# Performance work log

Hardware: AMD Instinct MI355X
Metric: run time of the kernel (lower is better)

## Reference

```python
import jax, jax.numpy as jnp
import numpy as np

B, P, PLOIDY = 8, 5000, 2
NALLELES, NPOS, D = 16, 20000, 64


def setup_inputs() -> dict:
    key = jax.random.key(0)
    k1, k2, k3, k4, k5 = jax.random.split(key, 5)
    alleles = jax.random.randint(k1, (B, P, PLOIDY), 0, NALLELES, dtype=jnp.int32)
    positions = jax.random.randint(k2, (B, P), 0, NPOS, dtype=jnp.int32)
    allele_table = jax.random.normal(k3, (NALLELES, D), dtype=jnp.float32)
    kernel_table = jax.random.normal(k4, (NPOS, D * D), dtype=jnp.float32)
    bias_table = jax.random.normal(k5, (NPOS, D), dtype=jnp.float32)
    return {"alleles": alleles, "positions": positions,
            "allele_table": allele_table, "kernel_table": kernel_table,
            "bias_table": bias_table}


def reference(alleles, positions, allele_table, kernel_table, bias_table):
    # gather allele embeddings and sum over ploidy: [B,P,ploidy,D] -> [B,P,D]
    a = allele_table[alleles].sum(axis=-2)
    # per-position weight matrix: [B,P,D,D]
    kernel = kernel_table[positions].reshape(positions.shape[0], positions.shape[1], D, D)
    bias = bias_table[positions]                       # [B,P,D]
    # batched 1xD @ DxD matmul, fused with bias add
    out = jnp.einsum('bpd,bpde->bpe', a, kernel) + bias
    return out  # activation is None (linear)
```

## Files before the change

### kernel.cpp

```cpp
#include <hip/hip_runtime.h>

#define BB 8
#define PP 5000
#define DD 64
#define NBP (BB * PP)
#define NPOSC 20000
#define SLOTS 16
#define GRID_POS (NPOSC / 4)

static __device__ __forceinline__ float4 f4add(float4 a, float4 b) {
    return make_float4(a.x + b.x, a.y + b.y, a.z + b.z, a.w + b.w);
}

__global__ __launch_bounds__(256) void claim_kernel(
    const int* __restrict__ positions,
    int* __restrict__ cnt,
    int* __restrict__ ovf_cnt,
    int* __restrict__ order2,
    int* __restrict__ ovf)
{
    const int tid = blockIdx.x * 256 + threadIdx.x;
    if (tid < NBP) {
        const int p = positions[tid];
        const int k = atomicAdd(&cnt[p], 1);
        if (k < SLOTS) order2[p * SLOTS + k] = tid;
        else           ovf[atomicAdd(ovf_cnt, 1)] = tid;
    }
}

__global__ __launch_bounds__(256) void allele_embed_kernel(
    const int* __restrict__ alleles,
    const float* __restrict__ allele_table,
    const float4* __restrict__ ktab4,
    const float4* __restrict__ btab4,
    const int* __restrict__ cnt,
    const int* __restrict__ order2,
    float4* __restrict__ out4)
{
    const int wave = threadIdx.x >> 6;
    const int lane = threadIdx.x & 63;
    const int work = (blockIdx.x & 7) * (GRID_POS / 8) + (blockIdx.x >> 3);
    const int pos  = work * 4 + wave;

    int n = cnt[pos];
    if (n == 0) return;
    if (n > SLOTS) n = SLOTS;

    const float4* __restrict__ krow = ktab4 + (size_t)pos * (DD * DD / 4);
    const int* __restrict__ slot = order2 + pos * SLOTS;
    const int dg = lane >> 4;
    const float4 bv = btab4[(size_t)pos * (DD / 4) + (lane & 15)];

    if (n == 1) {
        const int bp = slot[0];
        const float a = allele_table[alleles[bp * 2] * DD + lane]
                      + allele_table[alleles[bp * 2 + 1] * DD + lane];
        float4 acc = make_float4(0.f, 0.f, 0.f, 0.f);
#pragma unroll
        for (int i = 0; i < 16; ++i) {
            const float ad = __shfl(a, i * 4 + dg, 64);
            const float4 kv = krow[i * 64 + lane];
            acc.x += ad * kv.x; acc.y += ad * kv.y;
            acc.z += ad * kv.z; acc.w += ad * kv.w;
        }
#pragma unroll
        for (int off = 16; off <= 32; off <<= 1) {
            acc.x += __shfl_xor(acc.x, off, 64); acc.y += __shfl_xor(acc.y, off, 64);
            acc.z += __shfl_xor(acc.z, off, 64); acc.w += __shfl_xor(acc.w, off, 64);
        }
        if (lane < 16) out4[(size_t)bp * (DD / 4) + lane] = f4add(acc, bv);
        return;
    }

    for (int c = 0; c < n; c += 4) {
        const int m = n - c;
        const int bp0 = slot[c];
        const int bp1 = (m > 1) ? slot[c + 1] : bp0;
        const int bp2 = (m > 2) ? slot[c + 2] : bp0;
        const int bp3 = (m > 3) ? slot[c + 3] : bp0;

        const float a0 = allele_table[alleles[bp0 * 2] * DD + lane]
                       + allele_table[alleles[bp0 * 2 + 1] * DD + lane];
        const float a1 = allele_table[alleles[bp1 * 2] * DD + lane]
                       + allele_table[alleles[bp1 * 2 + 1] * DD + lane];
        const float a2 = allele_table[alleles[bp2 * 2] * DD + lane]
                       + allele_table[alleles[bp2 * 2 + 1] * DD + lane];
        const float a3 = allele_table[alleles[bp3 * 2] * DD + lane]
                       + allele_table[alleles[bp3 * 2 + 1] * DD + lane];

        float4 acc0 = make_float4(0.f, 0.f, 0.f, 0.f);
        float4 acc1 = acc0, acc2 = acc0, acc3 = acc0;
#pragma unroll
        for (int i = 0; i < 16; ++i) {
            const int d = i * 4 + dg;
            const float4 kv = krow[i * 64 + lane];
            const float d0 = __shfl(a0, d, 64);
            const float d1 = __shfl(a1, d, 64);
            const float d2 = __shfl(a2, d, 64);
            const float d3 = __shfl(a3, d, 64);
            acc0.x += d0 * kv.x; acc0.y += d0 * kv.y; acc0.z += d0 * kv.z; acc0.w += d0 * kv.w;
            acc1.x += d1 * kv.x; acc1.y += d1 * kv.y; acc1.z += d1 * kv.z; acc1.w += d1 * kv.w;
            acc2.x += d2 * kv.x; acc2.y += d2 * kv.y; acc2.z += d2 * kv.z; acc2.w += d2 * kv.w;
            acc3.x += d3 * kv.x; acc3.y += d3 * kv.y; acc3.z += d3 * kv.z; acc3.w += d3 * kv.w;
        }
#pragma unroll
        for (int off = 16; off <= 32; off <<= 1) {
            acc0.x += __shfl_xor(acc0.x, off, 64); acc0.y += __shfl_xor(acc0.y, off, 64);
            acc0.z += __shfl_xor(acc0.z, off, 64); acc0.w += __shfl_xor(acc0.w, off, 64);
            acc1.x += __shfl_xor(acc1.x, off, 64); acc1.y += __shfl_xor(acc1.y, off, 64);
            acc1.z += __shfl_xor(acc1.z, off, 64); acc1.w += __shfl_xor(acc1.w, off, 64);
            acc2.x += __shfl_xor(acc2.x, off, 64); acc2.y += __shfl_xor(acc2.y, off, 64);
            acc2.z += __shfl_xor(acc2.z, off, 64); acc2.w += __shfl_xor(acc2.w, off, 64);
            acc3.x += __shfl_xor(acc3.x, off, 64); acc3.y += __shfl_xor(acc3.y, off, 64);
            acc3.z += __shfl_xor(acc3.z, off, 64); acc3.w += __shfl_xor(acc3.w, off, 64);
        }
        if (lane < 16) {
            out4[(size_t)bp0 * (DD / 4) + lane] = f4add(acc0, bv);
            if (m > 1) out4[(size_t)bp1 * (DD / 4) + lane] = f4add(acc1, bv);
            if (m > 2) out4[(size_t)bp2 * (DD / 4) + lane] = f4add(acc2, bv);
            if (m > 3) out4[(size_t)bp3 * (DD / 4) + lane] = f4add(acc3, bv);
        }
    }
}

__global__ __launch_bounds__(256) void tail_kernel(
    const int* __restrict__ alleles,
    const int* __restrict__ positions,
    const float* __restrict__ allele_table,
    const float4* __restrict__ ktab4,
    const float4* __restrict__ btab4,
    const int* __restrict__ ovf_cnt,
    const int* __restrict__ ovf,
    float4* __restrict__ out4)
{
    const int nov  = *ovf_cnt;
    const int lane = threadIdx.x & 63;
    const int wid  = blockIdx.x * 4 + (threadIdx.x >> 6);
    const int dg   = lane >> 4;
    for (int i = wid; i < nov; i += 256) {
        const int bp  = ovf[i];
        const int pos = positions[bp];
        const float a = allele_table[alleles[bp * 2] * DD + lane]
                      + allele_table[alleles[bp * 2 + 1] * DD + lane];
        const float4* krow = ktab4 + (size_t)pos * (DD * DD / 4);
        float4 acc = make_float4(0.f, 0.f, 0.f, 0.f);
#pragma unroll
        for (int k = 0; k < 16; ++k) {
            const float ad = __shfl(a, k * 4 + dg, 64);
            const float4 kv = krow[k * 64 + lane];
            acc.x += ad * kv.x; acc.y += ad * kv.y;
            acc.z += ad * kv.z; acc.w += ad * kv.w;
        }
#pragma unroll
        for (int off = 16; off <= 32; off <<= 1) {
            acc.x += __shfl_xor(acc.x, off, 64); acc.y += __shfl_xor(acc.y, off, 64);
            acc.z += __shfl_xor(acc.z, off, 64); acc.w += __shfl_xor(acc.w, off, 64);
        }
        if (lane < 16) {
            const float4 bv = btab4[(size_t)pos * (DD / 4) + lane];
            out4[(size_t)bp * (DD / 4) + lane] = f4add(acc, bv);
        }
    }
}

extern "C" void kernel_launch(void* const* d_in, const int* in_sizes, int n_in,
                              void* d_out, int out_size, void* d_ws, size_t ws_size,
                              hipStream_t stream) {
    const int*   alleles      = (const int*)d_in[0];
    const int*   positions    = (const int*)d_in[1];
    const float* allele_table = (const float*)d_in[2];
    const float4* ktab4       = (const float4*)d_in[3];
    const float4* btab4       = (const float4*)d_in[4];
    float4* out4              = (float4*)d_out;

    int* cnt     = (int*)d_ws;
    int* ovf_cnt = cnt + NPOSC;
    int* order2  = cnt + NPOSC + 32;
    int* ovf     = order2 + NPOSC * SLOTS;

    hipMemsetAsync(cnt, 0, (NPOSC + 32) * sizeof(int), stream);

    const int gprep = (NBP + 255) / 256;
    claim_kernel<<<gprep, 256, 0, stream>>>(positions, cnt, ovf_cnt, order2, ovf);

    allele_embed_kernel<<<GRID_POS, 256, 0, stream>>>(
        alleles, allele_table, ktab4, btab4, cnt, order2, out4);

    tail_kernel<<<64, 256, 0, stream>>>(
        alleles, positions, allele_table, ktab4, btab4, ovf_cnt, ovf, out4);
}
```

Before: 442.6 us.

## Use nontemporal kernel-table loads and output stores, vector types, and paired claims

Streams the per-position weight rows and the output with nontemporal loads and stores so they bypass cache retention, and switches to native ext_vector float4 arithmetic. Reads the allele pairs as a single int2 load. The claim kernel now handles two positions per thread, and the tail kernel is shrunk to 16 blocks with a matching stride. Nontemporal hints may not help, because rows are reused within a position, and the smaller tail grid could serialize overflow work.

```diff
diff --git a/kernel.cpp b/kernel.cpp
--- a/kernel.cpp
+++ b/kernel.cpp
@@ -8,9 +8,7 @@
 #define SLOTS 16
 #define GRID_POS (NPOSC / 4)
 
-static __device__ __forceinline__ float4 f4add(float4 a, float4 b) {
-    return make_float4(a.x + b.x, a.y + b.y, a.z + b.z, a.w + b.w);
-}
+typedef float v4f __attribute__((ext_vector_type(4)));
 
 __global__ __launch_bounds__(256) void claim_kernel(
     const int* __restrict__ positions,
@@ -19,23 +17,30 @@
     int* __restrict__ order2,
     int* __restrict__ ovf)
 {
-    const int tid = blockIdx.x * 256 + threadIdx.x;
-    if (tid < NBP) {
-        const int p = positions[tid];
-        const int k = atomicAdd(&cnt[p], 1);
-        if (k < SLOTS) order2[p * SLOTS + k] = tid;
-        else           ovf[atomicAdd(ovf_cnt, 1)] = tid;
+    const int tid  = blockIdx.x * 256 + threadIdx.x;
+    const int base = tid * 2;
+    if (base >= NBP) return;
+    const int2 p2 = ((const int2*)positions)[tid];
+    {
+        const int k = atomicAdd(&cnt[p2.x], 1);
+        if (k < SLOTS) order2[p2.x * SLOTS + k] = base;
+        else           ovf[atomicAdd(ovf_cnt, 1)] = base;
+    }
+    {
+        const int k = atomicAdd(&cnt[p2.y], 1);
+        if (k < SLOTS) order2[p2.y * SLOTS + k] = base + 1;
+        else           ovf[atomicAdd(ovf_cnt, 1)] = base + 1;
     }
 }
 
 __global__ __launch_bounds__(256) void allele_embed_kernel(
-    const int* __restrict__ alleles,
+    const int2* __restrict__ all2,
     const float* __restrict__ allele_table,
-    const float4* __restrict__ ktab4,
-    const float4* __restrict__ btab4,
+    const v4f* __restrict__ ktab4,
+    const v4f* __restrict__ btab4,
     const int* __restrict__ cnt,
     const int* __restrict__ order2,
-    float4* __restrict__ out4)
+    v4f* __restrict__ out4)
 {
     const int wave = threadIdx.x >> 6;
     const int lane = threadIdx.x & 63;
@@ -46,29 +51,30 @@
     if (n == 0) return;
     if (n > SLOTS) n = SLOTS;
 
-    const float4* __restrict__ krow = ktab4 + (size_t)pos * (DD * DD / 4);
+    const v4f* __restrict__ krow = ktab4 + (size_t)pos * (DD * DD / 4);
     const int* __restrict__ slot = order2 + pos * SLOTS;
     const int dg = lane >> 4;
-    const float4 bv = btab4[(size_t)pos * (DD / 4) + (lane & 15)];
+    const v4f bv = btab4[(size_t)pos * (DD / 4) + (lane & 15)];
 
     if (n == 1) {
         const int bp = slot[0];
-        const float a = allele_table[alleles[bp * 2] * DD + lane]
-                      + allele_table[alleles[bp * 2 + 1] * DD + lane];
-        float4 acc = make_float4(0.f, 0.f, 0.f, 0.f);
+        const int2 al = all2[bp];
+        const float a = allele_table[al.x * DD + lane]
+                      + allele_table[al.y * DD + lane];
+        v4f acc = (v4f)(0.f);
 #pragma unroll
         for (int i = 0; i < 16; ++i) {
             const float ad = __shfl(a, i * 4 + dg, 64);
-            const float4 kv = krow[i * 64 + lane];
-            acc.x += ad * kv.x; acc.y += ad * kv.y;
-            acc.z += ad * kv.z; acc.w += ad * kv.w;
+            const v4f kv = __builtin_nontemporal_load(&krow[i * 64 + lane]);
+            acc += ad * kv;
         }
 #pragma unroll
         for (int off = 16; off <= 32; off <<= 1) {
             acc.x += __shfl_xor(acc.x, off, 64); acc.y += __shfl_xor(acc.y, off, 64);
             acc.z += __shfl_xor(acc.z, off, 64); acc.w += __shfl_xor(acc.w, off, 64);
         }
-        if (lane < 16) out4[(size_t)bp * (DD / 4) + lane] = f4add(acc, bv);
+        if (lane < 16)
+            __builtin_nontemporal_store(acc + bv, &out4[(size_t)bp * (DD / 4) + lane]);
         return;
     }
 
@@ -79,29 +85,21 @@
         const int bp2 = (m > 2) ? slot[c + 2] : bp0;
         const int bp3 = (m > 3) ? slot[c + 3] : bp0;
 
-        const float a0 = allele_table[alleles[bp0 * 2] * DD + lane]
-                       + allele_table[alleles[bp0 * 2 + 1] * DD + lane];
-        const float a1 = allele_table[alleles[bp1 * 2] * DD + lane]
-                       + allele_table[alleles[bp1 * 2 + 1] * DD + lane];
-        const float a2 = allele_table[alleles[bp2 * 2] * DD + lane]
-                       + allele_table[alleles[bp2 * 2 + 1] * DD + lane];
-        const float a3 = allele_table[alleles[bp3 * 2] * DD + lane]
-                       + allele_table[alleles[bp3 * 2 + 1] * DD + lane];
+        const int2 e0 = all2[bp0], e1 = all2[bp1], e2 = all2[bp2], e3 = all2[bp3];
+        const float a0 = allele_table[e0.x * DD + lane] + allele_table[e0.y * DD + lane];
+        const float a1 = allele_table[e1.x * DD + lane] + allele_table[e1.y * DD + lane];
+        const float a2 = allele_table[e2.x * DD + lane] + allele_table[e2.y * DD + lane];
+        const float a3 = allele_table[e3.x * DD + lane] + allele_table[e3.y * DD + lane];
 
-        float4 acc0 = make_float4(0.f, 0.f, 0.f, 0.f);
-        float4 acc1 = acc0, acc2 = acc0, acc3 = acc0;
+        v4f acc0 = (v4f)(0.f), acc1 = (v4f)(0.f), acc2 = (v4f)(0.f), acc3 = (v4f)(0.f);
 #pragma unroll
         for (int i = 0; i < 16; ++i) {
             const int d = i * 4 + dg;
-            const float4 kv = krow[i * 64 + lane];
-            const float d0 = __shfl(a0, d, 64);
-            const float d1 = __shfl(a1, d, 64);
-            const float d2 = __shfl(a2, d, 64);
-            const float d3 = __shfl(a3, d, 64);
-            acc0.x += d0 * kv.x; acc0.y += d0 * kv.y; acc0.z += d0 * kv.z; acc0.w += d0 * kv.w;
-            acc1.x += d1 * kv.x; acc1.y += d1 * kv.y; acc1.z += d1 * kv.z; acc1.w += d1 * kv.w;
-            acc2.x += d2 * kv.x; acc2.y += d2 * kv.y; acc2.z += d2 * kv.z; acc2.w += d2 * kv.w;
-            acc3.x += d3 * kv.x; acc3.y += d3 * kv.y; acc3.z += d3 * kv.z; acc3.w += d3 * kv.w;
+            const v4f kv = __builtin_nontemporal_load(&krow[i * 64 + lane]);
+            acc0 += __shfl(a0, d, 64) * kv;
+            acc1 += __shfl(a1, d, 64) * kv;
+            acc2 += __shfl(a2, d, 64) * kv;
+            acc3 += __shfl(a3, d, 64) * kv;
         }
 #pragma unroll
         for (int off = 16; off <= 32; off <<= 1) {
@@ -115,41 +113,40 @@
             acc3.z += __shfl_xor(acc3.z, off, 64); acc3.w += __shfl_xor(acc3.w, off, 64);
         }
         if (lane < 16) {
-            out4[(size_t)bp0 * (DD / 4) + lane] = f4add(acc0, bv);
-            if (m > 1) out4[(size_t)bp1 * (DD / 4) + lane] = f4add(acc1, bv);
-            if (m > 2) out4[(size_t)bp2 * (DD / 4) + lane] = f4add(acc2, bv);
-            if (m > 3) out4[(size_t)bp3 * (DD / 4) + lane] = f4add(acc3, bv);
+            __builtin_nontemporal_store(acc0 + bv, &out4[(size_t)bp0 * (DD / 4) + lane]);
+            if (m > 1) __builtin_nontemporal_store(acc1 + bv, &out4[(size_t)bp1 * (DD / 4) + lane]);
+            if (m > 2) __builtin_nontemporal_store(acc2 + bv, &out4[(size_t)bp2 * (DD / 4) + lane]);
+            if (m > 3) __builtin_nontemporal_store(acc3 + bv, &out4[(size_t)bp3 * (DD / 4) + lane]);
         }
     }
 }
 
 __global__ __launch_bounds__(256) void tail_kernel(
-    const int* __restrict__ alleles,
+    const int2* __restrict__ all2,
     const int* __restrict__ positions,
     const float* __restrict__ allele_table,
-    const float4* __restrict__ ktab4,
-    const float4* __restrict__ btab4,
+    const v4f* __restrict__ ktab4,
+    const v4f* __restrict__ btab4,
     const int* __restrict__ ovf_cnt,
     const int* __restrict__ ovf,
-    float4* __restrict__ out4)
+    v4f* __restrict__ out4)
 {
     const int nov  = *ovf_cnt;
     const int lane = threadIdx.x & 63;
     const int wid  = blockIdx.x * 4 + (threadIdx.x >> 6);
     const int dg   = lane >> 4;
-    for (int i = wid; i < nov; i += 256) {
+    for (int i = wid; i < nov; i += 64) {
         const int bp  = ovf[i];
         const int pos = positions[bp];
-        const float a = allele_table[alleles[bp * 2] * DD + lane]
-                      + allele_table[alleles[bp * 2 + 1] * DD + lane];
-        const float4* krow = ktab4 + (size_t)pos * (DD * DD / 4);
-        float4 acc = make_float4(0.f, 0.f, 0.f, 0.f);
+        const int2 al = all2[bp];
+        const float a = allele_table[al.x * DD + lane]
+                      + allele_table[al.y * DD + lane];
+        const v4f* krow = ktab4 + (size_t)pos * (DD * DD / 4);
+        v4f acc = (v4f)(0.f);
 #pragma unroll
         for (int k = 0; k < 16; ++k) {
             const float ad = __shfl(a, k * 4 + dg, 64);
-            const float4 kv = krow[k * 64 + lane];
-            acc.x += ad * kv.x; acc.y += ad * kv.y;
-            acc.z += ad * kv.z; acc.w += ad * kv.w;
+            acc += ad * krow[k * 64 + lane];
         }
 #pragma unroll
         for (int off = 16; off <= 32; off <<= 1) {
@@ -157,8 +154,8 @@
             acc.z += __shfl_xor(acc.z, off, 64); acc.w += __shfl_xor(acc.w, off, 64);
         }
         if (lane < 16) {
-            const float4 bv = btab4[(size_t)pos * (DD / 4) + lane];
-            out4[(size_t)bp * (DD / 4) + lane] = f4add(acc, bv);
+            const v4f bv = btab4[(size_t)pos * (DD / 4) + lane];
+            out4[(size_t)bp * (DD / 4) + lane] = acc + bv;
         }
     }
 }
@@ -169,9 +166,10 @@
     const int*   alleles      = (const int*)d_in[0];
     const int*   positions    = (const int*)d_in[1];
     const float* allele_table = (const float*)d_in[2];
-    const float4* ktab4       = (const float4*)d_in[3];
-    const float4* btab4       = (const float4*)d_in[4];
-    float4* out4              = (float4*)d_out;
+    const v4f*   ktab4        = (const v4f*)d_in[3];
+    const v4f*   btab4        = (const v4f*)d_in[4];
+    v4f* out4                 = (v4f*)d_out;
+    const int2* all2          = (const int2*)alleles;
 
     int* cnt     = (int*)d_ws;
     int* ovf_cnt = cnt + NPOSC;
@@ -180,12 +178,12 @@
 
     hipMemsetAsync(cnt, 0, (NPOSC + 32) * sizeof(int), stream);
 
-    const int gprep = (NBP + 255) / 256;
-    claim_kernel<<<gprep, 256, 0, stream>>>(positions, cnt, ovf_cnt, order2, ovf);
+    const int gclaim = (NBP / 2 + 255) / 256;
+    claim_kernel<<<gclaim, 256, 0, stream>>>(positions, cnt, ovf_cnt, order2, ovf);
 
     allele_embed_kernel<<<GRID_POS, 256, 0, stream>>>(
-        alleles, allele_table, ktab4, btab4, cnt, order2, out4);
+        all2, allele_table, ktab4, btab4, cnt, order2, out4);
 
-    tail_kernel<<<64, 256, 0, stream>>>(
-        alleles, positions, allele_table, ktab4, btab4, ovf_cnt, ovf, out4);
+    tail_kernel<<<16, 256, 0, stream>>>(
+        all2, positions, allele_table, ktab4, btab4, ovf_cnt, ovf, out4);
 }
```

After: 432.5 us. 1.02x faster.
